# Optimization experiments

Hardware: AMD Instinct MI355X
Metric: run time of the kernel (lower is better)

Reference implementation:

```python
import jax, jax.numpy as jnp
import numpy as np

HEADS = 8
DIM_HEAD = 64
SCALE = DIM_HEAD ** -0.5


def setup_inputs() -> dict:
    key = jax.random.key(0)
    ks = jax.random.split(key, 6)
    B, T, C, H, W = 16, 64, 512, 64, 64
    inner = HEADS * DIM_HEAD  # 512
    return {
        "vision_feature": jax.random.normal(ks[0], (B, C, H, W), jnp.float32),
        "language_feature": jax.random.normal(ks[1], (B, T, C), jnp.float32),
        "mask": jnp.ones((B, T), jnp.int32),  # unused by the module's forward
        "Wq": jax.random.normal(ks[2], (inner, C), jnp.float32) * (C ** -0.5),
        "Wk": jax.random.normal(ks[3], (inner, C), jnp.float32) * (C ** -0.5),
        "Wv": jax.random.normal(ks[4], (inner, C), jnp.float32) * (C ** -0.5),
        "Wo": jax.random.normal(ks[5], (C, inner), jnp.float32) * (inner ** -0.5),
    }


def reference(vision_feature, language_feature, mask, Wq, Wk, Wv, Wo):
    B, T, C = language_feature.shape
    _, _, H, W = vision_feature.shape
    S = H * W
    # 1x1 conv projections == matmuls over the channel dim
    q = jnp.einsum('btc,ic->bti', language_feature, Wq)           # (B, T, inner)
    vis = vision_feature.reshape(B, C, S)                          # (B, C, S)
    k = jnp.einsum('ic,bcs->bis', Wk, vis)                         # (B, inner, S)
    v = jnp.einsum('ic,bcs->bis', Wv, vis)                         # (B, inner, S)
    # split heads: channel index = n*dim_head + d  (n outermost)
    q = q.reshape(B, T, HEADS, DIM_HEAD).transpose(2, 0, 1, 3)     # (h, B, T, d)
    k = k.reshape(B, HEADS, DIM_HEAD, S).transpose(1, 0, 2, 3)     # (h, B, d, S)
    v = v.reshape(B, HEADS, DIM_HEAD, S).transpose(1, 0, 3, 2)     # (h, B, S, d)
    att = jax.nn.softmax(jnp.einsum('hbtd,hbds->hbts', q, k) * SCALE, axis=-1)
    out = jnp.einsum('hbts,hbsd->hbtd', att, v)                    # (h, B, T, d)
    # merge heads back: b (n c) tokens -> equivalently (B, T, h*d)
    out = out.transpose(1, 2, 0, 3).reshape(B, T, HEADS * DIM_HEAD)
    out = jnp.einsum('bti,oi->bto', out, Wo)                       # (B, T, C)
    return out
```

## Files before the change

### kernel.cpp

```cpp
#include <hip/hip_runtime.h>
#include <stdint.h>

typedef __attribute__((ext_vector_type(8))) short short8;
typedef __attribute__((ext_vector_type(4))) short short4v;
typedef __attribute__((ext_vector_type(4))) float float4v;
typedef __attribute__((ext_vector_type(8))) __bf16 bf16x8;

#define NCH 4

__device__ __forceinline__ float4v mfma16x16x32(short8 a, short8 b, float4v c) {
  return __builtin_amdgcn_mfma_f32_16x16x32_bf16(
      __builtin_bit_cast(bf16x8, a), __builtin_bit_cast(bf16x8, b), c, 0, 0, 0);
}

__device__ __forceinline__ short f2bf(float f) {
  uint32_t u = __builtin_bit_cast(uint32_t, f);
  u += 0x7fffu + ((u >> 16) & 1u);
  return (short)(u >> 16);
}

__device__ __forceinline__ float bf2f(short s) {
  return __builtin_bit_cast(float, ((uint32_t)(uint16_t)s) << 16);
}

__device__ __forceinline__ void load_lds16(const short* g, short* l) {
  __builtin_amdgcn_global_load_lds(
      (const __attribute__((address_space(1))) void*)g,
      (__attribute__((address_space(3))) void*)l, 16, 0, 0);
}

__global__ __launch_bounds__(256) void convert5(
    const float* __restrict__ sl, short* __restrict__ dl,
    const float* __restrict__ s1, short* __restrict__ d1,
    const float* __restrict__ s2, short* __restrict__ d2,
    const float* __restrict__ s3, short* __restrict__ d3,
    const float* __restrict__ s4, short* __restrict__ d4) {
  const float* src; short* dst; int n4;
  switch (blockIdx.y) {
    case 0: src = sl; dst = dl; n4 = 131072; break;
    case 1: src = s1; dst = d1; n4 = 65536; break;
    case 2: src = s2; dst = d2; n4 = 65536; break;
    case 3: src = s3; dst = d3; n4 = 65536; break;
    default: src = s4; dst = d4; n4 = 65536; break;
  }
  const int stride = gridDim.x * blockDim.x;
  for (int i = blockIdx.x * blockDim.x + threadIdx.x; i < n4; i += stride) {
    float4v v = *(const float4v*)(src + (long)i * 4);
    short4v o;
#pragma unroll
    for (int r = 0; r < 4; r++) o[r] = f2bf(v[r]);
    *(short4v*)(dst + (long)i * 4) = o;
  }
}

template <int OUT_F32>
__global__ __launch_bounds__(256) void gemm_nt(
    const short* __restrict__ A, const short* __restrict__ B,
    void* __restrict__ C, int K, int ldc, float scale) {
  __shared__ alignas(16) short lA[128 * 32];
  __shared__ alignas(16) short lB[128 * 32];
  const int tid = threadIdx.x;
  const int lane = tid & 63, w = tid >> 6;
  const int quad = lane >> 4, l16 = lane & 15;
  const int wm = w >> 1, wn = w & 1;
  const long m0 = (long)blockIdx.y * 128, n0 = (long)blockIdx.x * 128;

  float4v acc[4][4];
#pragma unroll
  for (int i = 0; i < 4; i++)
#pragma unroll
    for (int j = 0; j < 4; j++) acc[i][j] = (float4v)0.0f;

  const int srow = tid >> 2;
  const int scol = (((tid & 3) ^ ((srow >> 1) & 3))) * 8;

  load_lds16(&A[(m0 + srow) * K + scol], &lA[tid * 8]);
  load_lds16(&A[(m0 + 64 + srow) * K + scol], &lA[2048 + tid * 8]);
  load_lds16(&B[(n0 + srow) * K + scol], &lB[tid * 8]);
  load_lds16(&B[(n0 + 64 + srow) * K + scol], &lB[2048 + tid * 8]);

  for (int kt = 0; kt < K; kt += 32) {
    __syncthreads();

    short8 af[4], bf[4];
#pragma unroll
    for (int t = 0; t < 4; t++) {
      const int ra = wm * 64 + t * 16 + l16;
      const int rb = wn * 64 + t * 16 + l16;
      af[t] = *(const short8*)&lA[ra * 32 + ((quad ^ ((ra >> 1) & 3)) * 8)];
      bf[t] = *(const short8*)&lB[rb * 32 + ((quad ^ ((rb >> 1) & 3)) * 8)];
    }
    __syncthreads();

    if (kt + 32 < K) {
      load_lds16(&A[(m0 + srow) * K + kt + 32 + scol], &lA[tid * 8]);
      load_lds16(&A[(m0 + 64 + srow) * K + kt + 32 + scol], &lA[2048 + tid * 8]);
      load_lds16(&B[(n0 + srow) * K + kt + 32 + scol], &lB[tid * 8]);
      load_lds16(&B[(n0 + 64 + srow) * K + kt + 32 + scol], &lB[2048 + tid * 8]);
    }
#pragma unroll
    for (int i = 0; i < 4; i++)
#pragma unroll
      for (int j = 0; j < 4; j++)
        acc[i][j] = mfma16x16x32(af[i], bf[j], acc[i][j]);
  }

  const int cm = wm * 64 + quad * 4;
  const int cn = wn * 64 + l16;
  if (OUT_F32) {
    float* Cf = (float*)C;
#pragma unroll
    for (int i = 0; i < 4; i++)
#pragma unroll
      for (int j = 0; j < 4; j++) {
        const long gn = n0 + cn + j * 16;
#pragma unroll
        for (int r = 0; r < 4; r++)
          Cf[(m0 + cm + i * 16 + r) * (long)ldc + gn] = acc[i][j][r] * scale;
      }
  } else {
    short* Cs = (short*)C;
#pragma unroll
    for (int i = 0; i < 4; i++)
#pragma unroll
      for (int j = 0; j < 4; j++) {
        const long gn = n0 + cn + j * 16;
#pragma unroll
        for (int r = 0; r < 4; r++)
          Cs[(m0 + cm + i * 16 + r) * (long)ldc + gn] = f2bf(acc[i][j][r] * scale);
      }
  }
}

__global__ __launch_bounds__(512) void gemm_kv(
    const short* __restrict__ Wk, const short* __restrict__ Wv,
    const short* __restrict__ visT, long sV,
    short* __restrict__ kout, short* __restrict__ vout, long sKV) {
  __shared__ alignas(16) short smem[12288];
  short* lWk = smem;
  short* lWv = smem + 4096;
  short* lVis = smem + 8192;
  const int tid = threadIdx.x;
  const int lane = tid & 63, w = tid >> 6;
  const int quad = lane >> 4, l16 = lane & 15;
  const int role = w >> 2;
  const int wq = w & 3, wm = wq >> 1, wn = wq & 1;
  const long n0 = (long)blockIdx.x * 128;
  const long m0 = (long)blockIdx.y * 128;
  const short* vis = visT + blockIdx.z * sV;
  short* kz = kout + blockIdx.z * sKV;
  short* vz = vout + blockIdx.z * sKV;

  float4v acc[4][4];
#pragma unroll
  for (int i = 0; i < 4; i++)
#pragma unroll
    for (int j = 0; j < 4; j++) acc[i][j] = (float4v)0.0f;

  const int srow = tid >> 2;
  const int scol = (((tid & 3) ^ ((srow >> 1) & 3))) * 8;
  const short* lW = role ? lWv : lWk;

  load_lds16(&Wk[(m0 + srow) * 512 + scol], &lWk[tid * 8]);
  load_lds16(&Wv[(m0 + srow) * 512 + scol], &lWv[tid * 8]);
  load_lds16(&vis[(n0 + srow) * 512 + scol], &lVis[tid * 8]);

  for (int kt = 0; kt < 512; kt += 32) {
    __syncthreads();

    short8 af[4], bf[4];
#pragma unroll
    for (int t = 0; t < 4; t++) {
      const int ra = wm * 64 + t * 16 + l16;
      const int rb = wn * 64 + t * 16 + l16;
      af[t] = *(const short8*)&lW[ra * 32 + ((quad ^ ((ra >> 1) & 3)) * 8)];
      bf[t] = *(const short8*)&lVis[rb * 32 + ((quad ^ ((rb >> 1) & 3)) * 8)];
    }
    __syncthreads();

    if (kt + 32 < 512) {
      load_lds16(&Wk[(m0 + srow) * 512 + kt + 32 + scol], &lWk[tid * 8]);
      load_lds16(&Wv[(m0 + srow) * 512 + kt + 32 + scol], &lWv[tid * 8]);
      load_lds16(&vis[(n0 + srow) * 512 + kt + 32 + scol], &lVis[tid * 8]);
    }
#pragma unroll
    for (int i = 0; i < 4; i++)
#pragma unroll
      for (int j = 0; j < 4; j++)
        acc[i][j] = mfma16x16x32(af[i], bf[j], acc[i][j]);
  }

  const int cm = wm * 64 + quad * 4;
  const int cn = wn * 64 + l16;

  if (role == 1) {
#pragma unroll
    for (int i = 0; i < 4; i++)
#pragma unroll
      for (int j = 0; j < 4; j++) {
        const long gn = n0 + cn + j * 16;
#pragma unroll
        for (int r = 0; r < 4; r++)
          vz[(m0 + cm + i * 16 + r) * 4096 + gn] = f2bf(acc[i][j][r]);
      }
  }

  short* scratch = smem;
#pragma unroll
  for (int h = 0; h < 2; h++) {
    __syncthreads();
    if (role == 0 && wn == h) {
#pragma unroll
      for (int j = 0; j < 4; j++)
#pragma unroll
        for (int i = 0; i < 4; i++) {
          const int nloc = j * 16 + l16;
          const int m = wm * 64 + i * 16 + quad * 4;
          short4v pk;
#pragma unroll
          for (int r = 0; r < 4; r++) pk[r] = f2bf(acc[i][j][r]);
          *(short4v*)&scratch[nloc * 136 + m] = pk;
        }
    }
    __syncthreads();
    {
      const int row = tid >> 3;
      const int off = (tid & 7) * 16;
      short8 v0 = *(const short8*)&scratch[row * 136 + off];
      short8 v1 = *(const short8*)&scratch[row * 136 + off + 8];
      *(short8*)&kz[(n0 + h * 64 + row) * 512 + m0 + off] = v0;
      *(short8*)&kz[(n0 + h * 64 + row) * 512 + m0 + off + 8] = v1;
    }
  }
}

__global__ __launch_bounds__(256) void transpose_f2b(
    const float* __restrict__ vis, short* __restrict__ visT) {
  __shared__ alignas(16) short buf[64][68];
  const int tid = threadIdx.x;
  const long bz = blockIdx.z;
  const long s0 = (long)blockIdx.x * 64;
  const long c0 = (long)blockIdx.y * 64;
  const float* src = vis + bz * 512 * 4096;
  short* dst = visT + bz * 4096 * 512;
  const int tr = tid >> 4;
  const int tc4 = (tid & 15) * 4;
#pragma unroll
  for (int i = 0; i < 4; i++) {
    const int c = tr + i * 16;
    float4v val = *(const float4v*)&src[(c0 + c) * 4096 + s0 + tc4];
    buf[tc4 + 0][c] = f2bf(val[0]);
    buf[tc4 + 1][c] = f2bf(val[1]);
    buf[tc4 + 2][c] = f2bf(val[2]);
    buf[tc4 + 3][c] = f2bf(val[3]);
  }
  __syncthreads();
#pragma unroll
  for (int i = 0; i < 4; i++) {
    const int s = tr + i * 16;
    short4v val = *(const short4v*)&buf[s][tc4];
    *(short4v*)&dst[(s0 + s) * 512 + c0 + tc4] = val;
  }
}

__global__ __launch_bounds__(256) void attn_part(
    const short* __restrict__ q, const short* __restrict__ kws,
    const short* __restrict__ vws, float* __restrict__ Opart,
    float* __restrict__ lpart, int b0) {
  const int h = blockIdx.x;
  const int bz = blockIdx.y;
  const int ch = blockIdx.z;
  const int tid = threadIdx.x;
  const int lane = tid & 63, w = tid >> 6;
  const int quad = lane >> 4, l16 = lane & 15;

  __shared__ alignas(16) short lq[64 * 64];
  __shared__ alignas(16) short lk[128 * 64];
  __shared__ alignas(16) short lv[64 * 128];
  __shared__ alignas(16) short lp[64 * 128];
  __shared__ float lsum[64];

  const short* qb = q + ((long)(b0 + bz) * 64) * 512 + h * 64;
  const short* kb = kws + (long)bz * 4096 * 512 + h * 64;
  const short* vb = vws + (long)bz * 512 * 4096 + (long)h * 64 * 4096;

  if (tid < 64) lsum[tid] = 0.0f;
  {
    const int qr = tid >> 3;
    const int qc = ((tid & 7) ^ (qr & 7)) * 8;
    load_lds16(&qb[qr * 512 + qc], &lq[tid * 8]);
    load_lds16(&qb[(32 + qr) * 512 + qc], &lq[2048 + tid * 8]);
  }
  const int s0_first = ch * (4096 / NCH);
  const int send = s0_first + (4096 / NCH);
#pragma unroll
  for (int it = 0; it < 4; it++) {
    const int li = tid + it * 256;
    const int kr = li >> 3;
    const int kc = ((li & 7) ^ (kr & 7)) * 8;
    load_lds16(&kb[(long)(s0_first + kr) * 512 + kc], &lk[li * 8]);
  }
#pragma unroll
  for (int it = 0; it < 4; it++) {
    const int li = tid + it * 256;
    const int vr = li >> 4;
    const int vc = ((li & 15) ^ (vr & 7)) * 8;
    load_lds16(&vb[(long)vr * 4096 + s0_first + vc], &lv[li * 8]);
  }
  __syncthreads();

  short8 aq[4][2];
#pragma unroll
  for (int mt = 0; mt < 4; mt++)
#pragma unroll
    for (int ks = 0; ks < 2; ks++) {
      const int ra = mt * 16 + l16;
      aq[mt][ks] = *(const short8*)&lq[ra * 64 + (((ks * 4 + quad) ^ (ra & 7)) * 8)];
    }

  float4v osc[4];
#pragma unroll
  for (int mt = 0; mt < 4; mt++) osc[mt] = (float4v)0.0f;
  float lrow[4][4] = {};

  for (int s0 = s0_first; s0 < send; s0 += 128) {
    short8 bk[2][2];
#pragma unroll
    for (int ks = 0; ks < 2; ks++)
#pragma unroll
      for (int jn = 0; jn < 2; jn++) {
        const int rb = (2 * w + jn) * 16 + l16;
        bk[ks][jn] = *(const short8*)&lk[rb * 64 + (((ks * 4 + quad) ^ (rb & 7)) * 8)];
      }
    short8 bv[4];
#pragma unroll
    for (int ks = 0; ks < 4; ks++) {
      const int rv = w * 16 + l16;
      bv[ks] = *(const short8*)&lv[rv * 128 + (((ks * 4 + quad) ^ (rv & 7)) * 8)];
    }
    __syncthreads();

    if (s0 + 128 < send) {
#pragma unroll
      for (int it = 0; it < 4; it++) {
        const int li = tid + it * 256;
        const int kr = li >> 3;
        const int kc = ((li & 7) ^ (kr & 7)) * 8;
        load_lds16(&kb[(long)(s0 + 128 + kr) * 512 + kc], &lk[li * 8]);
      }
#pragma unroll
      for (int it = 0; it < 4; it++) {
        const int li = tid + it * 256;
        const int vr = li >> 4;
        const int vc = ((li & 15) ^ (vr & 7)) * 8;
        load_lds16(&vb[(long)vr * 4096 + s0 + 128 + vc], &lv[li * 8]);
      }
    }

    float4v sc[4][2];
#pragma unroll
    for (int mt = 0; mt < 4; mt++)
#pragma unroll
      for (int jn = 0; jn < 2; jn++) sc[mt][jn] = (float4v)0.0f;
#pragma unroll
    for (int ks = 0; ks < 2; ks++)
#pragma unroll
      for (int mt = 0; mt < 4; mt++)
#pragma unroll
        for (int jn = 0; jn < 2; jn++)
          sc[mt][jn] = mfma16x16x32(aq[mt][ks], bk[ks][jn], sc[mt][jn]);

#pragma unroll
    for (int mt = 0; mt < 4; mt++)
#pragma unroll
      for (int jn = 0; jn < 2; jn++)
#pragma unroll
        for (int r = 0; r < 4; r++) {
          const float scv = fminf(fmaxf(sc[mt][jn][r], -80.0f), 30.0f);
          const short sp = f2bf(__expf(scv));
          lrow[mt][r] += bf2f(sp);
          const int rowp = mt * 16 + quad * 4 + r;
          const int col = (2 * w + jn) * 16 + l16;
          lp[rowp * 128 + (((col >> 3) ^ (rowp & 7)) * 8) + (col & 7)] = sp;
        }
    __syncthreads();

#pragma unroll
    for (int ks = 0; ks < 4; ks++)
#pragma unroll
      for (int mt = 0; mt < 4; mt++) {
        const int rp = mt * 16 + l16;
        const short8 ap = *(const short8*)&lp[rp * 128 + (((ks * 4 + quad) ^ (rp & 7)) * 8)];
        osc[mt] = mfma16x16x32(ap, bv[ks], osc[mt]);
      }
    __syncthreads();
  }

#pragma unroll
  for (int mt = 0; mt < 4; mt++)
#pragma unroll
    for (int r = 0; r < 4; r++) {
      float v = lrow[mt][r];
      v += __shfl_xor(v, 1);
      v += __shfl_xor(v, 2);
      v += __shfl_xor(v, 4);
      v += __shfl_xor(v, 8);
      if (l16 == 0) atomicAdd(&lsum[mt * 16 + quad * 4 + r], v);
    }
  __syncthreads();

  const long bh = bz * 8 + h;
  float* op = Opart + ((bh * NCH + ch) * 64) * 64 + w * 16 + l16;
#pragma unroll
  for (int mt = 0; mt < 4; mt++)
#pragma unroll
    for (int r = 0; r < 4; r++)
      op[(long)(mt * 16 + quad * 4 + r) * 64] = osc[mt][r];
  if (tid < 64) lpart[(bh * NCH + ch) * 64 + tid] = lsum[tid];
}

__global__ __launch_bounds__(256) void attn_combine(
    const float* __restrict__ Opart, const float* __restrict__ lpart,
    short* __restrict__ tmp, int b0, int nbh) {
  const int total = nbh * 4096;
  for (int idx = blockIdx.x * 256 + threadIdx.x; idx < total;
       idx += gridDim.x * 256) {
    const int bh = idx >> 12;
    const int td = idx & 4095;
    const int t = td >> 6, d = td & 63;
    float o = 0.0f, l = 0.0f;
#pragma unroll
    for (int c = 0; c < NCH; c++) {
      o += Opart[((long)bh * NCH + c) * 4096 + td];
      l += lpart[(bh * NCH + c) * 64 + t];
    }
    const int b = b0 + (bh >> 3), h = bh & 7;
    tmp[((long)b * 64 + t) * 512 + h * 64 + d] = f2bf(o / l);
  }
}

extern "C" void kernel_launch(void* const* d_in, const int* in_sizes, int n_in,
                              void* d_out, int out_size, void* d_ws, size_t ws_size,
                              hipStream_t stream) {
  (void)in_sizes; (void)n_in; (void)out_size;
  const float* vis = (const float*)d_in[0];
  const float* lang = (const float*)d_in[1];
  const float* Wq = (const float*)d_in[3];
  const float* Wk = (const float*)d_in[4];
  const float* Wv = (const float*)d_in[5];
  const float* Wo = (const float*)d_in[6];
  float* out = (float*)d_out;

  char* ws = (char*)d_ws;
  const size_t MB = 1 << 20;
  short* q_ws = (short*)(ws + 0 * MB);
  short* tmp_ws = (short*)(ws + 1 * MB);
  short* langb = (short*)(ws + 2 * MB);
  short* Wqb = (short*)(ws + 3 * MB);
  short* Wkb = (short*)(ws + 3 * MB + 512 * 1024);
  short* Wvb = (short*)(ws + 4 * MB);
  short* Wob = (short*)(ws + 4 * MB + 512 * 1024);
  char* grp = ws + 5 * MB;

  const long batch_elems = 4096l * 512;
  int g = 16;
  const int cands[5] = {1, 2, 4, 8, 16};
  for (int ci = 0; ci < 5; ci++) {
    const size_t need = 5 * MB + 3ull * (16 / cands[ci]) * batch_elems * 2;
    if (need <= ws_size) { g = cands[ci]; break; }
  }
  const int Bg = 16 / g;
  short* visT = (short*)grp;
  short* k_ws = visT + (long)Bg * batch_elems;
  short* v_ws = k_ws + (long)Bg * batch_elems;
  float* Opart = (float*)visT;
  float* lptr = Opart + (long)Bg * 8 * NCH * 4096;

  convert5<<<dim3(128, 5), 256, 0, stream>>>(lang, langb, Wq, Wqb, Wk, Wkb,
                                             Wv, Wvb, Wo, Wob);

  gemm_nt<0><<<dim3(4, 8), 256, 0, stream>>>(langb, Wqb, q_ws, 512, 512, 0.125f);

  for (int gi = 0; gi < g; gi++) {
    const int b0 = gi * Bg;
    transpose_f2b<<<dim3(64, 8, Bg), 256, 0, stream>>>(vis + (long)b0 * batch_elems, visT);
    gemm_kv<<<dim3(32, 4, Bg), 512, 0, stream>>>(Wkb, Wvb, visT, batch_elems,
                                                 k_ws, v_ws, batch_elems);
    attn_part<<<dim3(8, Bg, NCH), 256, 0, stream>>>(q_ws, k_ws, v_ws, Opart, lptr, b0);
    attn_combine<<<512, 256, 0, stream>>>(Opart, lptr, tmp_ws, b0, Bg * 8);
  }

  gemm_nt<1><<<dim3(4, 8), 256, 0, stream>>>(tmp_ws, Wob, out, 512, 512, 1.0f);
}
```

Before: 379.5 us.

## Double-buffer LDS tiles in GEMM kernels with explicit vmcnt waits

Converts gemm_nt and gemm_kv from a single LDS buffer to a two-stage ping-pong buffer. Tile t+2 is prefetched while tile t is computed, and a partial s_waitcnt vmcnt lets the next tile's loads stay in flight across the barrier. Some __syncthreads are replaced with explicit lgkmcnt waits plus raw s_barrier, and the attention kernel gets the same barrier treatment. This doubles LDS use per block, which may lower occupancy, and it relies on exact hand-counted vmcnt values.

```diff
diff --git a/kernel.cpp b/kernel.cpp
--- a/kernel.cpp
+++ b/kernel.cpp
@@ -57,8 +57,7 @@
 __global__ __launch_bounds__(256) void gemm_nt(
     const short* __restrict__ A, const short* __restrict__ B,
     void* __restrict__ C, int K, int ldc, float scale) {
-  __shared__ alignas(16) short lA[128 * 32];
-  __shared__ alignas(16) short lB[128 * 32];
+  __shared__ alignas(16) short smem[16384];
   const int tid = threadIdx.x;
   const int lane = tid & 63, w = tid >> 6;
   const int quad = lane >> 4, l16 = lane & 15;
@@ -73,15 +72,30 @@
 
   const int srow = tid >> 2;
   const int scol = (((tid & 3) ^ ((srow >> 1) & 3))) * 8;
-
-  load_lds16(&A[(m0 + srow) * K + scol], &lA[tid * 8]);
-  load_lds16(&A[(m0 + 64 + srow) * K + scol], &lA[2048 + tid * 8]);
-  load_lds16(&B[(n0 + srow) * K + scol], &lB[tid * 8]);
-  load_lds16(&B[(n0 + 64 + srow) * K + scol], &lB[2048 + tid * 8]);
-
-  for (int kt = 0; kt < K; kt += 32) {
-    __syncthreads();
-
+  const int nit = K >> 5;
+
+#define STAGE_NT(t, base)                                                       \
+  do {                                                                          \
+    load_lds16(&A[(m0 + srow) * K + (t) * 32 + scol], &smem[(base) + tid * 8]); \
+    load_lds16(&A[(m0 + 64 + srow) * K + (t) * 32 + scol],                      \
+               &smem[(base) + 2048 + tid * 8]);                                 \
+    load_lds16(&B[(n0 + srow) * K + (t) * 32 + scol],                           \
+               &smem[(base) + 4096 + tid * 8]);                                 \
+    load_lds16(&B[(n0 + 64 + srow) * K + (t) * 32 + scol],                      \
+               &smem[(base) + 6144 + tid * 8]);                                 \
+  } while (0)
+
+  STAGE_NT(0, 0);
+  if (nit > 1) STAGE_NT(1, 8192);
+
+  for (int it = 0; it < nit; ++it) {
+    const int base = (it & 1) * 8192;
+    if (it + 1 < nit) asm volatile("s_waitcnt vmcnt(4)" ::: "memory");
+    else              asm volatile("s_waitcnt vmcnt(0)" ::: "memory");
+    __builtin_amdgcn_s_barrier();
+
+    const short* lA = &smem[base];
+    const short* lB = &smem[base + 4096];
     short8 af[4], bf[4];
 #pragma unroll
     for (int t = 0; t < 4; t++) {
@@ -90,20 +104,18 @@
       af[t] = *(const short8*)&lA[ra * 32 + ((quad ^ ((ra >> 1) & 3)) * 8)];
       bf[t] = *(const short8*)&lB[rb * 32 + ((quad ^ ((rb >> 1) & 3)) * 8)];
     }
-    __syncthreads();
-
-    if (kt + 32 < K) {
-      load_lds16(&A[(m0 + srow) * K + kt + 32 + scol], &lA[tid * 8]);
-      load_lds16(&A[(m0 + 64 + srow) * K + kt + 32 + scol], &lA[2048 + tid * 8]);
-      load_lds16(&B[(n0 + srow) * K + kt + 32 + scol], &lB[tid * 8]);
-      load_lds16(&B[(n0 + 64 + srow) * K + kt + 32 + scol], &lB[2048 + tid * 8]);
-    }
+    asm volatile("s_waitcnt lgkmcnt(0)" ::: "memory");
+    __builtin_amdgcn_sched_barrier(0);
+    __builtin_amdgcn_s_barrier();
+
+    if (it + 2 < nit) STAGE_NT(it + 2, base);
 #pragma unroll
     for (int i = 0; i < 4; i++)
 #pragma unroll
       for (int j = 0; j < 4; j++)
         acc[i][j] = mfma16x16x32(af[i], bf[j], acc[i][j]);
   }
+#undef STAGE_NT
 
   const int cm = wm * 64 + quad * 4;
   const int cn = wn * 64 + l16;
@@ -136,10 +148,7 @@
     const short* __restrict__ Wk, const short* __restrict__ Wv,
     const short* __restrict__ visT, long sV,
     short* __restrict__ kout, short* __restrict__ vout, long sKV) {
-  __shared__ alignas(16) short smem[12288];
-  short* lWk = smem;
-  short* lWv = smem + 4096;
-  short* lVis = smem + 8192;
+  __shared__ alignas(16) short smem[24576];
   const int tid = threadIdx.x;
   const int lane = tid & 63, w = tid >> 6;
   const int quad = lane >> 4, l16 = lane & 15;
@@ -159,15 +168,29 @@
 
   const int srow = tid >> 2;
   const int scol = (((tid & 3) ^ ((srow >> 1) & 3))) * 8;
-  const short* lW = role ? lWv : lWk;
-
-  load_lds16(&Wk[(m0 + srow) * 512 + scol], &lWk[tid * 8]);
-  load_lds16(&Wv[(m0 + srow) * 512 + scol], &lWv[tid * 8]);
-  load_lds16(&vis[(n0 + srow) * 512 + scol], &lVis[tid * 8]);
-
-  for (int kt = 0; kt < 512; kt += 32) {
-    __syncthreads();
-
+
+  const short* gWk = &Wk[(m0 + srow) * 512 + scol];
+  const short* gWv = &Wv[(m0 + srow) * 512 + scol];
+  const short* gV = &vis[(n0 + srow) * 512 + scol];
+
+#define STAGE_KV(t, base)                                      \
+  do {                                                         \
+    load_lds16(gWk + (t) * 32, &smem[(base) + tid * 8]);       \
+    load_lds16(gWv + (t) * 32, &smem[(base) + 4096 + tid * 8]);\
+    load_lds16(gV + (t) * 32, &smem[(base) + 8192 + tid * 8]); \
+  } while (0)
+
+  STAGE_KV(0, 0);
+  STAGE_KV(1, 12288);
+
+  for (int it = 0; it < 16; ++it) {
+    const int base = (it & 1) * 12288;
+    if (it < 15) asm volatile("s_waitcnt vmcnt(3)" ::: "memory");
+    else         asm volatile("s_waitcnt vmcnt(0)" ::: "memory");
+    __builtin_amdgcn_s_barrier();
+
+    const short* lW = &smem[base + (role ? 4096 : 0)];
+    const short* lVis = &smem[base + 8192];
     short8 af[4], bf[4];
 #pragma unroll
     for (int t = 0; t < 4; t++) {
@@ -176,19 +199,18 @@
       af[t] = *(const short8*)&lW[ra * 32 + ((quad ^ ((ra >> 1) & 3)) * 8)];
       bf[t] = *(const short8*)&lVis[rb * 32 + ((quad ^ ((rb >> 1) & 3)) * 8)];
     }
-    __syncthreads();
-
-    if (kt + 32 < 512) {
-      load_lds16(&Wk[(m0 + srow) * 512 + kt + 32 + scol], &lWk[tid * 8]);
-      load_lds16(&Wv[(m0 + srow) * 512 + kt + 32 + scol], &lWv[tid * 8]);
-      load_lds16(&vis[(n0 + srow) * 512 + kt + 32 + scol], &lVis[tid * 8]);
-    }
+    asm volatile("s_waitcnt lgkmcnt(0)" ::: "memory");
+    __builtin_amdgcn_sched_barrier(0);
+    __builtin_amdgcn_s_barrier();
+
+    if (it + 2 < 16) STAGE_KV(it + 2, base);
 #pragma unroll
     for (int i = 0; i < 4; i++)
 #pragma unroll
       for (int j = 0; j < 4; j++)
         acc[i][j] = mfma16x16x32(af[i], bf[j], acc[i][j]);
   }
+#undef STAGE_KV
 
   const int cm = wm * 64 + quad * 4;
   const int cn = wn * 64 + l16;
@@ -383,7 +405,9 @@
           const int col = (2 * w + jn) * 16 + l16;
           lp[rowp * 128 + (((col >> 3) ^ (rowp & 7)) * 8) + (col & 7)] = sp;
         }
-    __syncthreads();
+    asm volatile("s_waitcnt lgkmcnt(0)" ::: "memory");
+    __builtin_amdgcn_sched_barrier(0);
+    __builtin_amdgcn_s_barrier();
 
 #pragma unroll
     for (int ks = 0; ks < 4; ks++)
```

Result: faster. 349.4 us (-7.9%).
